# Kernel tuning notes

Hardware: AMD Instinct MI355X
Metric: run time of the kernel (lower is better)

The kernel has to match this reference:

```python
import jax, jax.numpy as jnp
import numpy as np

B, N, E, H = 2, 2048, 1024, 16
D = E // H  # head_dim = 64


def setup_inputs() -> dict:
    key = jax.random.key(0)
    ks = jax.random.split(key, 8)
    s = 1.0 / np.sqrt(D)
    return {
        "query": jax.random.normal(ks[0], (B, N, E), jnp.float32),
        "key": jax.random.normal(ks[1], (B, N, E), jnp.float32),
        "value": jax.random.normal(ks[2], (B, N, E), jnp.float32),
        "mask": jax.random.randint(ks[3], (B, N), 0, 2, jnp.int32),
        # per-head Linear weights, torch layout (out_features, in_features) stacked over heads
        "Wq": jax.random.uniform(ks[4], (H, D, D), jnp.float32, -s, s),
        "Wk": jax.random.uniform(ks[5], (H, D, D), jnp.float32, -s, s),
        "Wv": jax.random.uniform(ks[6], (H, D, D), jnp.float32, -s, s),
        "Wo": jax.random.uniform(ks[7], (E, E), jnp.float32, -1.0 / np.sqrt(E), 1.0 / np.sqrt(E)),
    }


def reference(query, key, value, mask, Wq, Wk, Wv, Wo):
    b, n, e = query.shape
    h, d, _ = Wq.shape
    q = query.reshape(b, n, h, d)
    k = key.reshape(b, n, h, d)
    v = value.reshape(b, n, h, d)
    # per-head Linear (no bias): x @ W[i].T, batched over heads
    qh = jnp.einsum('bnhd,hed->bnhe', q, Wq)
    kh = jnp.einsum('bnhd,hed->bnhe', k, Wk)
    vh = jnp.einsum('bnhd,hed->bnhe', v, Wv)
    # NOTE: original scales by sqrt(embed_size), not sqrt(head_dim)
    scores = jnp.einsum('bqhd,bkhd->bhqk', qh, kh) / (e ** 0.5)
    # NOTE: mask is unsqueezed on the KEY axis position in torch (dim=2),
    # so it masks entire QUERY rows, broadcasting over keys.
    scores = jnp.where(mask[:, None, :, None] == 0, jnp.float32(-1e28), scores)
    probs = jax.nn.softmax(scores, axis=-1)
    attn = jnp.einsum('bhqk,bkhd->bqhd', probs, vh).reshape(b, n, e)
    return attn @ Wo.T
```

## Files before the change

kernel.cpp:

```cpp
#include <hip/hip_runtime.h>
#include <hip/hip_bf16.h>

#define B_ 2
#define N_ 2048
#define E_ 1024
#define H_ 16
#define D_ 64
#define BH_ (B_ * H_)

typedef __attribute__((ext_vector_type(4))) float f32x4;
typedef __attribute__((ext_vector_type(8))) short bf16x8;
typedef __attribute__((ext_vector_type(4))) short s16x4;
typedef __attribute__((ext_vector_type(4))) int i32x4;
typedef __attribute__((ext_vector_type(2))) int i32x2;

#define MFMA(a, b, c) __builtin_amdgcn_mfma_f32_16x16x32_bf16(a, b, c, 0, 0, 0)

#define AS1(p) ((const __attribute__((address_space(1))) unsigned int*)(p))
#define AS3(p) ((__attribute__((address_space(3))) unsigned int*)(p))

static __device__ __forceinline__ unsigned short f2bf(float f) {
    unsigned int u = __builtin_bit_cast(unsigned int, f);
    u += 0x7fff + ((u >> 16) & 1);
    return (unsigned short)(u >> 16);
}
static __device__ __forceinline__ int pack2bf(float lo, float hi) {
    __hip_bfloat162 t = __float22bfloat162_rn(float2{lo, hi});
    int r;
    __builtin_memcpy(&r, &t, 4);
    return r;
}
static __device__ __forceinline__ bf16x8 cvt8s(const float* __restrict__ p, float sc) {
    f32x4 a = *(const f32x4*)p;
    f32x4 b = *(const f32x4*)(p + 4);
    i32x4 r = {pack2bf(a.x * sc, a.y * sc), pack2bf(a.z * sc, a.w * sc),
               pack2bf(b.x * sc, b.y * sc), pack2bf(b.z * sc, b.w * sc)};
    return __builtin_bit_cast(bf16x8, r);
}

__global__ __launch_bounds__(256, 4)
void proj_kernel(const float* __restrict__ q, const float* __restrict__ k,
                 const float* __restrict__ v,
                 const float* __restrict__ Wq, const float* __restrict__ Wk,
                 const float* __restrict__ Wv,
                 const int* __restrict__ mask,
                 unsigned short* __restrict__ qh, unsigned short* __restrict__ kh,
                 unsigned short* __restrict__ vt) {
    const int z = blockIdx.z;
    const float* X = (z == 0) ? q : (z == 1) ? k : v;
    const float* W = (z == 0) ? Wq : (z == 1) ? Wk : Wv;
    unsigned short* out = (z == 0) ? qh : (z == 1) ? kh : vt;
    const float wscale = (z == 0) ? (1.44269504f * 0.03125f) : 1.0f;

    const int lane = threadIdx.x & 63;
    const int wave = threadIdx.x >> 6;
    const int l16  = lane & 15;
    const int quad = lane >> 4;
    const int bh = blockIdx.y;
    const int b = bh >> 4, h = bh & 15;
    const int n0 = blockIdx.x * 64;
    const int tok = n0 + wave * 16 + l16;

    const float* xrow = X + ((size_t)(b * N_ + tok)) * E_ + h * 64;
    bf16x8 xf[2];
    xf[0] = cvt8s(xrow + quad * 8, 1.0f);
    xf[1] = cvt8s(xrow + 32 + quad * 8, 1.0f);

    const float* Wh = W + (size_t)h * 64 * 64;
    bf16x8 wf[4][2];
#pragma unroll
    for (int t4 = 0; t4 < 4; ++t4) {
        const float* wrow = Wh + (t4 * 16 + l16) * 64;
        wf[t4][0] = cvt8s(wrow + quad * 8, wscale);
        wf[t4][1] = cvt8s(wrow + 32 + quad * 8, wscale);
    }

    const int mk = (z == 0) ? mask[b * N_ + tok] : 1;

#pragma unroll
    for (int mi = 0; mi < 4; ++mi) {
        f32x4 a = {0.f, 0.f, 0.f, 0.f};
        a = MFMA(wf[mi][0], xf[0], a);
        a = MFMA(wf[mi][1], xf[1], a);
        if (z != 2) {
            i32x2 pk = {pack2bf(a.x, a.y), pack2bf(a.z, a.w)};
            if (!mk) pk = (i32x2){0, 0};
            *(i32x2*)(out + ((size_t)bh * N_ + tok) * 64 + mi * 16 + quad * 4) = pk;
        } else {
#pragma unroll
            for (int r = 0; r < 4; ++r) {
                int dout = mi * 16 + quad * 4 + r;
                out[((size_t)bh * 64 + dout) * N_ + tok] = (unsigned short)f2bf(a[r]);
            }
        }
    }
}

__global__ __launch_bounds__(256)
void cvt_wo_kernel(const float* __restrict__ wo, unsigned short* __restrict__ wob) {
    int idx = blockIdx.x * 256 + threadIdx.x;
    f32x4 v = *(const f32x4*)(wo + (size_t)idx * 4);
    i32x2 r = {pack2bf(v.x, v.y), pack2bf(v.z, v.w)};
    *(i32x2*)(wob + (size_t)idx * 4) = r;
}

__global__ __launch_bounds__(256, 2)
void attn_kernel(const unsigned short* __restrict__ qh,
                 const unsigned short* __restrict__ kh,
                 const unsigned short* __restrict__ vt,
                 unsigned short* __restrict__ attnb) {
    __shared__ short Kb[2][64][72];
    __shared__ short Vb[3][64][72];

    const int tid  = threadIdx.x;
    const int lane = tid & 63;
    const int wave = tid >> 6;
    const int l16  = lane & 15;
    const int quad = lane >> 4;

    const int flat = blockIdx.y * gridDim.x + blockIdx.x;
    const int qblk = flat >> 5;
    const int rem  = flat & 31;
    const int bh   = ((rem & 7) << 2) | (rem >> 3);
    const int b = bh >> 4, h = bh & 15;
    const int q0 = qblk * 128 + wave * 32;

    const unsigned short* kbase = kh + (size_t)bh * N_ * 64;
    const unsigned short* vbase = vt + (size_t)bh * 64 * N_;

    const int c0i = tid;
    const int c1i = tid + 256;
    const int o0 = (c0i >> 3) * 72 + (c0i & 7) * 8;
    const int o1 = (c1i >> 3) * 72 + (c1i & 7) * 8;

    short* kcur  = &Kb[0][0][0];
    short* knext = &Kb[1][0][0];
    short* vprev = &Vb[2][0][0];
    short* vcur  = &Vb[0][0][0];
    short* vnext = &Vb[1][0][0];

    const int srcA = (((quad * 2) & 3) << 4) + l16;
    const int srcB = (((quad * 2 + 1) & 3) << 4) + l16;
    const bool hiSel = (quad >= 2);

    bf16x8 qf[2][2];
#pragma unroll
    for (int qi = 0; qi < 2; ++qi) {
        const unsigned short* qrow = qh + ((size_t)bh * N_ + q0 + qi * 16 + l16) * 64;
        qf[qi][0] = *(const bf16x8*)(qrow + quad * 8);
        qf[qi][1] = *(const bf16x8*)(qrow + 32 + quad * 8);
    }

    float lI[2] = {0.f, 0.f};
    f32x4 o[4][2];
#pragma unroll
    for (int mi = 0; mi < 4; ++mi)
#pragma unroll
        for (int qi = 0; qi < 2; ++qi) o[mi][qi] = (f32x4){0.f, 0.f, 0.f, 0.f};

    bf16x8 pb[2][2];

    bf16x8 gK0, gK1, gV0, gV1;
    gK0 = *(const bf16x8*)(kbase + c0i * 8);
    gK1 = *(const bf16x8*)(kbase + c1i * 8);
    gV0 = *(const bf16x8*)(vbase + (size_t)(c0i >> 3) * N_ + (c0i & 7) * 8);
    gV1 = *(const bf16x8*)(vbase + (size_t)(c1i >> 3) * N_ + (c1i & 7) * 8);
    *(bf16x8*)(kcur + o0) = gK0;
    *(bf16x8*)(kcur + o1) = gK1;
    *(bf16x8*)(vcur + o0) = gV0;
    *(bf16x8*)(vcur + o1) = gV1;
    __syncthreads();

    for (int kt = 0; kt < N_ / 64; ++kt) {
        if (kt + 1 < N_ / 64) {
            const int k0n = (kt + 1) * 64;
            gK0 = *(const bf16x8*)(kbase + (size_t)k0n * 64 + c0i * 8);
            gK1 = *(const bf16x8*)(kbase + (size_t)k0n * 64 + c1i * 8);
            gV0 = *(const bf16x8*)(vbase + (size_t)(c0i >> 3) * N_ + k0n + (c0i & 7) * 8);
            gV1 = *(const bf16x8*)(vbase + (size_t)(c1i >> 3) * N_ + k0n + (c1i & 7) * 8);
        }

        bf16x8 ka[4][2];
#pragma unroll
        for (int t4 = 0; t4 < 4; ++t4) {
            ka[t4][0] = *(const bf16x8*)(kcur + (t4 * 16 + l16) * 72 + quad * 8);
            ka[t4][1] = *(const bf16x8*)(kcur + (t4 * 16 + l16) * 72 + 32 + quad * 8);
        }

        f32x4 s[2][4];
#pragma unroll
        for (int qi = 0; qi < 2; ++qi)
#pragma unroll
            for (int t4 = 0; t4 < 4; ++t4) {
                f32x4 z = {0.f, 0.f, 0.f, 0.f};
                z = MFMA(ka[t4][0], qf[qi][0], z);
                z = MFMA(ka[t4][1], qf[qi][1], z);
                s[qi][t4] = z;
            }

        if (kt > 0) {
            bf16x8 va[4][2];
#pragma unroll
            for (int mi = 0; mi < 4; ++mi) {
                va[mi][0] = *(const bf16x8*)(vprev + (mi * 16 + l16) * 72 + quad * 8);
                va[mi][1] = *(const bf16x8*)(vprev + (mi * 16 + l16) * 72 + 32 + quad * 8);
            }
#pragma unroll
            for (int mi = 0; mi < 4; ++mi)
#pragma unroll
                for (int qi = 0; qi < 2; ++qi) {
                    o[mi][qi] = MFMA(va[mi][0], pb[qi][0], o[mi][qi]);
                    o[mi][qi] = MFMA(va[mi][1], pb[qi][1], o[mi][qi]);
                }
        }

#pragma unroll
        for (int qi = 0; qi < 2; ++qi) {
            float rsum = 0.f;
            int pk[4][2];
#pragma unroll
            for (int t4 = 0; t4 < 4; ++t4) {
                f32x4 p;
#pragma unroll
                for (int r = 0; r < 4; ++r) {
                    p[r] = __builtin_amdgcn_exp2f(s[qi][t4][r]);
                    rsum += p[r];
                }
                pk[t4][0] = pack2bf(p.x, p.y);
                pk[t4][1] = pack2bf(p.z, p.w);
            }
            rsum += __shfl_xor(rsum, 16);
            rsum += __shfl_xor(rsum, 32);
            lI[qi] += rsum;

            i32x4 w0, w1;
#pragma unroll
            for (int d = 0; d < 2; ++d) {
                int a0 = __shfl(pk[0][d], srcA), a1 = __shfl(pk[1][d], srcA);
                int b0 = __shfl(pk[0][d], srcB), b1 = __shfl(pk[1][d], srcB);
                w0[d]     = hiSel ? a1 : a0;
                w0[2 + d] = hiSel ? b1 : b0;
                int c0 = __shfl(pk[2][d], srcA), c1 = __shfl(pk[3][d], srcA);
                int e0 = __shfl(pk[2][d], srcB), e1 = __shfl(pk[3][d], srcB);
                w1[d]     = hiSel ? c1 : c0;
                w1[2 + d] = hiSel ? e1 : e0;
            }
            pb[qi][0] = __builtin_bit_cast(bf16x8, w0);
            pb[qi][1] = __builtin_bit_cast(bf16x8, w1);
        }

        if (kt + 1 < N_ / 64) {
            *(bf16x8*)(knext + o0) = gK0;
            *(bf16x8*)(knext + o1) = gK1;
            *(bf16x8*)(vnext + o0) = gV0;
            *(bf16x8*)(vnext + o1) = gV1;
            __syncthreads();
        }

        short* t = kcur; kcur = knext; knext = t;
        short* tv = vprev; vprev = vcur; vcur = vnext; vnext = tv;
    }

    {
        bf16x8 va[4][2];
#pragma unroll
        for (int mi = 0; mi < 4; ++mi) {
            va[mi][0] = *(const bf16x8*)(vprev + (mi * 16 + l16) * 72 + quad * 8);
            va[mi][1] = *(const bf16x8*)(vprev + (mi * 16 + l16) * 72 + 32 + quad * 8);
        }
#pragma unroll
        for (int mi = 0; mi < 4; ++mi)
#pragma unroll
            for (int qi = 0; qi < 2; ++qi) {
                o[mi][qi] = MFMA(va[mi][0], pb[qi][0], o[mi][qi]);
                o[mi][qi] = MFMA(va[mi][1], pb[qi][1], o[mi][qi]);
            }
    }

#pragma unroll
    for (int qi = 0; qi < 2; ++qi) {
        const float inv = 1.0f / lI[qi];
        const int qrow_idx = q0 + qi * 16 + l16;
#pragma unroll
        for (int mi = 0; mi < 4; ++mi) {
            f32x4 ov = o[mi][qi];
            i32x2 pkk = {pack2bf(ov.x * inv, ov.y * inv),
                         pack2bf(ov.z * inv, ov.w * inv)};
            int d0 = mi * 16 + quad * 4;
            *(i32x2*)(attnb + ((size_t)(b * N_ + qrow_idx)) * E_ + h * 64 + d0) = pkk;
        }
    }
}

__global__ __launch_bounds__(512, 1)
void out_gemm_kernel(const unsigned short* __restrict__ A,
                     const unsigned short* __restrict__ Bw,
                     float* __restrict__ out) {
    __shared__ short As[2][128 * 32];
    __shared__ short Bs[2][128 * 32];

    const int tid  = threadIdx.x;
    const int lane = tid & 63;
    const int l16  = lane & 15;
    const int quad = lane >> 4;
    const int wave = tid >> 6;
    const int wm = wave & 1, wn = wave >> 1;
    const int m0 = blockIdx.x * 128;
    const int n0 = blockIdx.y * 128;

    const unsigned short* gA = A + (size_t)m0 * E_;
    const unsigned short* gB = Bw + (size_t)n0 * E_;

    f32x4 acc[4][2];
#pragma unroll
    for (int mt = 0; mt < 4; ++mt)
#pragma unroll
        for (int nt = 0; nt < 2; ++nt) acc[mt][nt] = (f32x4){0.f, 0.f, 0.f, 0.f};

    const int cc = tid >> 7, rr = tid & 127;
#define OG_STAGE(buf, k0)                                                        \
    {                                                                            \
        __builtin_amdgcn_global_load_lds(AS1(gA + (size_t)rr * E_ + (k0) + cc * 8), \
                                         AS3(&As[buf][tid * 8]), 16, 0, 0);      \
        __builtin_amdgcn_global_load_lds(AS1(gB + (size_t)rr * E_ + (k0) + cc * 8), \
                                         AS3(&Bs[buf][tid * 8]), 16, 0, 0);      \
    }

    OG_STAGE(0, 0)
    __syncthreads();

    for (int kt = 0; kt < E_ / 32; ++kt) {
        const int cur = kt & 1;
        if (kt + 1 < E_ / 32) OG_STAGE(cur ^ 1, (kt + 1) * 32)

        bf16x8 af[4], bf[2];
#pragma unroll
        for (int mt = 0; mt < 4; ++mt)
            af[mt] = *(const bf16x8*)(&As[cur][(quad * 128 + wm * 64 + mt * 16 + l16) * 8]);
#pragma unroll
        for (int nt = 0; nt < 2; ++nt)
            bf[nt] = *(const bf16x8*)(&Bs[cur][(quad * 128 + wn * 32 + nt * 16 + l16) * 8]);

#pragma unroll
        for (int mt = 0; mt < 4; ++mt)
#pragma unroll
            for (int nt = 0; nt < 2; ++nt)
                acc[mt][nt] = MFMA(af[mt], bf[nt], acc[mt][nt]);

        __syncthreads();
    }

#pragma unroll
    for (int mt = 0; mt < 4; ++mt)
#pragma unroll
        for (int nt = 0; nt < 2; ++nt)
#pragma unroll
            for (int r = 0; r < 4; ++r)
                out[(size_t)(m0 + wm * 64 + mt * 16 + quad * 4 + r) * E_ +
                    n0 + wn * 32 + nt * 16 + l16] = acc[mt][nt][r];
#undef OG_STAGE
}

extern "C" void kernel_launch(void* const* d_in, const int* in_sizes, int n_in,
                              void* d_out, int out_size, void* d_ws, size_t ws_size,
                              hipStream_t stream) {
    const float* q    = (const float*)d_in[0];
    const float* k    = (const float*)d_in[1];
    const float* v    = (const float*)d_in[2];
    const int*   mask = (const int*)d_in[3];
    const float* Wq   = (const float*)d_in[4];
    const float* Wk   = (const float*)d_in[5];
    const float* Wv   = (const float*)d_in[6];
    const float* Wo   = (const float*)d_in[7];
    float* out = (float*)d_out;

    char* ws = (char*)d_ws;
    unsigned short* qh    = (unsigned short*)(ws);
    unsigned short* kh    = (unsigned short*)(ws + (size_t)8 * 1024 * 1024);
    unsigned short* vt    = (unsigned short*)(ws + (size_t)16 * 1024 * 1024);
    unsigned short* attnb = (unsigned short*)(ws + (size_t)24 * 1024 * 1024);
    unsigned short* wob   = (unsigned short*)(ws);

    dim3 blk(256);
    proj_kernel<<<dim3(N_ / 64, BH_, 3), blk, 0, stream>>>(q, k, v, Wq, Wk, Wv, mask,
                                                           qh, kh, vt);
    attn_kernel<<<dim3(16, 32), blk, 0, stream>>>(qh, kh, vt, attnb);
    cvt_wo_kernel<<<dim3(E_ * E_ / 1024), blk, 0, stream>>>(Wo, wob);
    out_gemm_kernel<<<dim3(32, 8), dim3(512), 0, stream>>>(attnb, wob, out);
}
```

Measured before the change: 222.3 us.

## Load K and V fragments directly from global memory, dropping LDS staging

Removes the shared-memory K/V tiles and the per-iteration __syncthreads. Each wave now loads its MFMA fragments straight from global memory, prefetching the next K tile into registers. The software pipeline that deferred the PV product by one iteration is also removed, so PV runs in the same iteration. This cuts LDS traffic and block barriers, but each of the four waves now fetches the same K/V data separately from global/L2. The V loads are strided by N and now sit on the critical path inside the iteration.

```diff
diff --git a/kernel.cpp b/kernel.cpp
--- a/kernel.cpp
+++ b/kernel.cpp
@@ -109,9 +109,6 @@
                  const unsigned short* __restrict__ kh,
                  const unsigned short* __restrict__ vt,
                  unsigned short* __restrict__ attnb) {
-    __shared__ short Kb[2][64][72];
-    __shared__ short Vb[3][64][72];
-
     const int tid  = threadIdx.x;
     const int lane = tid & 63;
     const int wave = tid >> 6;
@@ -125,19 +122,8 @@
     const int b = bh >> 4, h = bh & 15;
     const int q0 = qblk * 128 + wave * 32;
 
-    const unsigned short* kbase = kh + (size_t)bh * N_ * 64;
-    const unsigned short* vbase = vt + (size_t)bh * 64 * N_;
-
-    const int c0i = tid;
-    const int c1i = tid + 256;
-    const int o0 = (c0i >> 3) * 72 + (c0i & 7) * 8;
-    const int o1 = (c1i >> 3) * 72 + (c1i & 7) * 8;
-
-    short* kcur  = &Kb[0][0][0];
-    short* knext = &Kb[1][0][0];
-    short* vprev = &Vb[2][0][0];
-    short* vcur  = &Vb[0][0][0];
-    short* vnext = &Vb[1][0][0];
+    const unsigned short* kp = kh + (size_t)bh * N_ * 64 + l16 * 64 + quad * 8;
+    const unsigned short* vp = vt + (size_t)bh * 64 * N_ + (size_t)l16 * N_ + quad * 8;
 
     const int srcA = (((quad * 2) & 3) << 4) + l16;
     const int srcB = (((quad * 2 + 1) & 3) << 4) + l16;
@@ -158,33 +144,30 @@
 #pragma unroll
         for (int qi = 0; qi < 2; ++qi) o[mi][qi] = (f32x4){0.f, 0.f, 0.f, 0.f};
 
-    bf16x8 pb[2][2];
-
-    bf16x8 gK0, gK1, gV0, gV1;
-    gK0 = *(const bf16x8*)(kbase + c0i * 8);
-    gK1 = *(const bf16x8*)(kbase + c1i * 8);
-    gV0 = *(const bf16x8*)(vbase + (size_t)(c0i >> 3) * N_ + (c0i & 7) * 8);
-    gV1 = *(const bf16x8*)(vbase + (size_t)(c1i >> 3) * N_ + (c1i & 7) * 8);
-    *(bf16x8*)(kcur + o0) = gK0;
-    *(bf16x8*)(kcur + o1) = gK1;
-    *(bf16x8*)(vcur + o0) = gV0;
-    *(bf16x8*)(vcur + o1) = gV1;
-    __syncthreads();
+    bf16x8 ka[4][2];
+#pragma unroll
+    for (int t4 = 0; t4 < 4; ++t4) {
+        ka[t4][0] = *(const bf16x8*)(kp + (size_t)(t4 * 16) * 64);
+        ka[t4][1] = *(const bf16x8*)(kp + (size_t)(t4 * 16) * 64 + 32);
+    }
 
     for (int kt = 0; kt < N_ / 64; ++kt) {
+        bf16x8 kan[4][2];
         if (kt + 1 < N_ / 64) {
-            const int k0n = (kt + 1) * 64;
-            gK0 = *(const bf16x8*)(kbase + (size_t)k0n * 64 + c0i * 8);
-            gK1 = *(const bf16x8*)(kbase + (size_t)k0n * 64 + c1i * 8);
-            gV0 = *(const bf16x8*)(vbase + (size_t)(c0i >> 3) * N_ + k0n + (c0i & 7) * 8);
-            gV1 = *(const bf16x8*)(vbase + (size_t)(c1i >> 3) * N_ + k0n + (c1i & 7) * 8);
-        }
-
-        bf16x8 ka[4][2];
-#pragma unroll
-        for (int t4 = 0; t4 < 4; ++t4) {
-            ka[t4][0] = *(const bf16x8*)(kcur + (t4 * 16 + l16) * 72 + quad * 8);
-            ka[t4][1] = *(const bf16x8*)(kcur + (t4 * 16 + l16) * 72 + 32 + quad * 8);
+            const unsigned short* kpn = kp + (size_t)(kt + 1) * 64 * 64;
+#pragma unroll
+            for (int t4 = 0; t4 < 4; ++t4) {
+                kan[t4][0] = *(const bf16x8*)(kpn + (size_t)(t4 * 16) * 64);
+                kan[t4][1] = *(const bf16x8*)(kpn + (size_t)(t4 * 16) * 64 + 32);
+            }
+        }
+
+        bf16x8 va[4][2];
+#pragma unroll
+        for (int mi = 0; mi < 4; ++mi) {
+            const unsigned short* vrow = vp + (size_t)(mi * 16) * N_ + kt * 64;
+            va[mi][0] = *(const bf16x8*)(vrow);
+            va[mi][1] = *(const bf16x8*)(vrow + 32);
         }
 
         f32x4 s[2][4];
@@ -197,22 +180,6 @@
                 z = MFMA(ka[t4][1], qf[qi][1], z);
                 s[qi][t4] = z;
             }
-
-        if (kt > 0) {
-            bf16x8 va[4][2];
-#pragma unroll
-            for (int mi = 0; mi < 4; ++mi) {
-                va[mi][0] = *(const bf16x8*)(vprev + (mi * 16 + l16) * 72 + quad * 8);
-                va[mi][1] = *(const bf16x8*)(vprev + (mi * 16 + l16) * 72 + 32 + quad * 8);
-            }
-#pragma unroll
-            for (int mi = 0; mi < 4; ++mi)
-#pragma unroll
-                for (int qi = 0; qi < 2; ++qi) {
-                    o[mi][qi] = MFMA(va[mi][0], pb[qi][0], o[mi][qi]);
-                    o[mi][qi] = MFMA(va[mi][1], pb[qi][1], o[mi][qi]);
-                }
-        }
 
 #pragma unroll
         for (int qi = 0; qi < 2; ++qi) {
@@ -245,36 +212,21 @@
                 w1[d]     = hiSel ? c1 : c0;
                 w1[2 + d] = hiSel ? e1 : e0;
             }
-            pb[qi][0] = __builtin_bit_cast(bf16x8, w0);
-            pb[qi][1] = __builtin_bit_cast(bf16x8, w1);
-        }
-
-        if (kt + 1 < N_ / 64) {
-            *(bf16x8*)(knext + o0) = gK0;
-            *(bf16x8*)(knext + o1) = gK1;
-            *(bf16x8*)(vnext + o0) = gV0;
-            *(bf16x8*)(vnext + o1) = gV1;
-            __syncthreads();
-        }
-
-        short* t = kcur; kcur = knext; knext = t;
-        short* tv = vprev; vprev = vcur; vcur = vnext; vnext = tv;
-    }
-
-    {
-        bf16x8 va[4][2];
-#pragma unroll
-        for (int mi = 0; mi < 4; ++mi) {
-            va[mi][0] = *(const bf16x8*)(vprev + (mi * 16 + l16) * 72 + quad * 8);
-            va[mi][1] = *(const bf16x8*)(vprev + (mi * 16 + l16) * 72 + 32 + quad * 8);
-        }
-#pragma unroll
-        for (int mi = 0; mi < 4; ++mi)
-#pragma unroll
-            for (int qi = 0; qi < 2; ++qi) {
-                o[mi][qi] = MFMA(va[mi][0], pb[qi][0], o[mi][qi]);
-                o[mi][qi] = MFMA(va[mi][1], pb[qi][1], o[mi][qi]);
-            }
+            bf16x8 pb0 = __builtin_bit_cast(bf16x8, w0);
+            bf16x8 pb1 = __builtin_bit_cast(bf16x8, w1);
+
+#pragma unroll
+            for (int mi = 0; mi < 4; ++mi) {
+                o[mi][qi] = MFMA(va[mi][0], pb0, o[mi][qi]);
+                o[mi][qi] = MFMA(va[mi][1], pb1, o[mi][qi]);
+            }
+        }
+
+#pragma unroll
+        for (int t4 = 0; t4 < 4; ++t4) {
+            ka[t4][0] = kan[t4][0];
+            ka[t4][1] = kan[t4][1];
+        }
     }
 
 #pragma unroll
```

New measurement: 275.0 us. 1.24x slower.

## Use fp16 16x16x16 MFMA for PV to drop cross-lane P shuffles

Applied to the files above, without the earlier changes.

Stores V transposed in fp16 and switches the P·V product to the 16x16x16 f16 MFMA, whose operand layout matches the score accumulator layout. This removes the per-tile __shfl permutation of probabilities. The row-sum reduction is deferred to the end, accumulating per-lane vectors. The change doubles the PV MFMA instruction count at half the K-depth, pads the V LDS rows to 76 and uses round-toward-zero fp16 conversion for P, which changes precision slightly.

```diff
diff --git a/kernel.cpp b/kernel.cpp
--- a/kernel.cpp
+++ b/kernel.cpp
@@ -13,8 +13,10 @@
 typedef __attribute__((ext_vector_type(4))) short s16x4;
 typedef __attribute__((ext_vector_type(4))) int i32x4;
 typedef __attribute__((ext_vector_type(2))) int i32x2;
+typedef __attribute__((ext_vector_type(4))) _Float16 f16x4;
 
 #define MFMA(a, b, c) __builtin_amdgcn_mfma_f32_16x16x32_bf16(a, b, c, 0, 0, 0)
+#define MFMA16(a, b, c) __builtin_amdgcn_mfma_f32_16x16x16f16(a, b, c, 0, 0, 0)
 
 #define AS1(p) ((const __attribute__((address_space(1))) unsigned int*)(p))
 #define AS3(p) ((__attribute__((address_space(3))) unsigned int*)(p))
@@ -36,6 +38,14 @@
     i32x4 r = {pack2bf(a.x * sc, a.y * sc), pack2bf(a.z * sc, a.w * sc),
                pack2bf(b.x * sc, b.y * sc), pack2bf(b.z * sc, b.w * sc)};
     return __builtin_bit_cast(bf16x8, r);
+}
+static __device__ __forceinline__ f16x4 pack4f16(f32x4 p) {
+    auto lo = __builtin_amdgcn_cvt_pkrtz(p.x, p.y);
+    auto hi = __builtin_amdgcn_cvt_pkrtz(p.z, p.w);
+    f16x4 r;
+    __builtin_memcpy(&r, &lo, 4);
+    __builtin_memcpy(((char*)&r) + 4, &hi, 4);
+    return r;
 }
 
 __global__ __launch_bounds__(256, 4)
@@ -90,7 +100,10 @@
 #pragma unroll
             for (int r = 0; r < 4; ++r) {
                 int dout = mi * 16 + quad * 4 + r;
-                out[((size_t)bh * 64 + dout) * N_ + tok] = (unsigned short)f2bf(a[r]);
+                _Float16 hv = (_Float16)a[r];
+                unsigned short us;
+                __builtin_memcpy(&us, &hv, 2);
+                out[((size_t)bh * 64 + dout) * N_ + tok] = us;
             }
         }
     }
@@ -109,8 +122,8 @@
                  const unsigned short* __restrict__ kh,
                  const unsigned short* __restrict__ vt,
                  unsigned short* __restrict__ attnb) {
-    __shared__ short Kb[2][64][72];
-    __shared__ short Vb[3][64][72];
+    __shared__ short Kb[2][64 * 72];
+    __shared__ short Vb[3][64 * 76];
 
     const int tid  = threadIdx.x;
     const int lane = tid & 63;
@@ -130,18 +143,16 @@
 
     const int c0i = tid;
     const int c1i = tid + 256;
-    const int o0 = (c0i >> 3) * 72 + (c0i & 7) * 8;
-    const int o1 = (c1i >> 3) * 72 + (c1i & 7) * 8;
-
-    short* kcur  = &Kb[0][0][0];
-    short* knext = &Kb[1][0][0];
-    short* vprev = &Vb[2][0][0];
-    short* vcur  = &Vb[0][0][0];
-    short* vnext = &Vb[1][0][0];
-
-    const int srcA = (((quad * 2) & 3) << 4) + l16;
-    const int srcB = (((quad * 2 + 1) & 3) << 4) + l16;
-    const bool hiSel = (quad >= 2);
+    const int k0o = (c0i >> 3) * 72 + (c0i & 7) * 8;
+    const int k1o = (c1i >> 3) * 72 + (c1i & 7) * 8;
+    const int v0o = (c0i >> 3) * 76 + (c0i & 7) * 8;
+    const int v1o = (c1i >> 3) * 76 + (c1i & 7) * 8;
+
+    short* kcur  = &Kb[0][0];
+    short* knext = &Kb[1][0];
+    short* vprev = &Vb[2][0];
+    short* vcur  = &Vb[0][0];
+    short* vnext = &Vb[1][0];
 
     bf16x8 qf[2][2];
 #pragma unroll
@@ -151,24 +162,24 @@
         qf[qi][1] = *(const bf16x8*)(qrow + 32 + quad * 8);
     }
 
-    float lI[2] = {0.f, 0.f};
+    f32x4 psum[2] = {{0.f, 0.f, 0.f, 0.f}, {0.f, 0.f, 0.f, 0.f}};
     f32x4 o[4][2];
 #pragma unroll
     for (int mi = 0; mi < 4; ++mi)
 #pragma unroll
         for (int qi = 0; qi < 2; ++qi) o[mi][qi] = (f32x4){0.f, 0.f, 0.f, 0.f};
 
-    bf16x8 pb[2][2];
+    f16x4 pf[2][4];
 
     bf16x8 gK0, gK1, gV0, gV1;
     gK0 = *(const bf16x8*)(kbase + c0i * 8);
     gK1 = *(const bf16x8*)(kbase + c1i * 8);
     gV0 = *(const bf16x8*)(vbase + (size_t)(c0i >> 3) * N_ + (c0i & 7) * 8);
     gV1 = *(const bf16x8*)(vbase + (size_t)(c1i >> 3) * N_ + (c1i & 7) * 8);
-    *(bf16x8*)(kcur + o0) = gK0;
-    *(bf16x8*)(kcur + o1) = gK1;
-    *(bf16x8*)(vcur + o0) = gV0;
-    *(bf16x8*)(vcur + o1) = gV1;
+    *(bf16x8*)(kcur + k0o) = gK0;
+    *(bf16x8*)(kcur + k1o) = gK1;
+    *(bf16x8*)(vcur + v0o) = gV0;
+    *(bf16x8*)(vcur + v1o) = gV1;
     __syncthreads();
 
     for (int kt = 0; kt < N_ / 64; ++kt) {
@@ -186,7 +197,6 @@
             ka[t4][0] = *(const bf16x8*)(kcur + (t4 * 16 + l16) * 72 + quad * 8);
             ka[t4][1] = *(const bf16x8*)(kcur + (t4 * 16 + l16) * 72 + 32 + quad * 8);
         }
-
         f32x4 s[2][4];
 #pragma unroll
         for (int qi = 0; qi < 2; ++qi)
@@ -199,61 +209,36 @@
             }
 
         if (kt > 0) {
-            bf16x8 va[4][2];
 #pragma unroll
             for (int mi = 0; mi < 4; ++mi) {
-                va[mi][0] = *(const bf16x8*)(vprev + (mi * 16 + l16) * 72 + quad * 8);
-                va[mi][1] = *(const bf16x8*)(vprev + (mi * 16 + l16) * 72 + 32 + quad * 8);
+#pragma unroll
+                for (int t4 = 0; t4 < 4; ++t4) {
+                    f16x4 va = *(const f16x4*)(vprev + (mi * 16 + l16) * 76 +
+                                               t4 * 16 + quad * 4);
+#pragma unroll
+                    for (int qi = 0; qi < 2; ++qi)
+                        o[mi][qi] = MFMA16(va, pf[qi][t4], o[mi][qi]);
+                }
             }
-#pragma unroll
-            for (int mi = 0; mi < 4; ++mi)
-#pragma unroll
-                for (int qi = 0; qi < 2; ++qi) {
-                    o[mi][qi] = MFMA(va[mi][0], pb[qi][0], o[mi][qi]);
-                    o[mi][qi] = MFMA(va[mi][1], pb[qi][1], o[mi][qi]);
-                }
         }
 
 #pragma unroll
         for (int qi = 0; qi < 2; ++qi) {
-            float rsum = 0.f;
-            int pk[4][2];
 #pragma unroll
             for (int t4 = 0; t4 < 4; ++t4) {
                 f32x4 p;
 #pragma unroll
-                for (int r = 0; r < 4; ++r) {
-                    p[r] = __builtin_amdgcn_exp2f(s[qi][t4][r]);
-                    rsum += p[r];
-                }
-                pk[t4][0] = pack2bf(p.x, p.y);
-                pk[t4][1] = pack2bf(p.z, p.w);
+                for (int r = 0; r < 4; ++r) p[r] = __builtin_amdgcn_exp2f(s[qi][t4][r]);
+                psum[qi] += p;
+                pf[qi][t4] = pack4f16(p);
             }
-            rsum += __shfl_xor(rsum, 16);
-            rsum += __shfl_xor(rsum, 32);
-            lI[qi] += rsum;
-
-            i32x4 w0, w1;
-#pragma unroll
-            for (int d = 0; d < 2; ++d) {
-                int a0 = __shfl(pk[0][d], srcA), a1 = __shfl(pk[1][d], srcA);
-                int b0 = __shfl(pk[0][d], srcB), b1 = __shfl(pk[1][d], srcB);
-                w0[d]     = hiSel ? a1 : a0;
-                w0[2 + d] = hiSel ? b1 : b0;
-                int c0 = __shfl(pk[2][d], srcA), c1 = __shfl(pk[3][d], srcA);
-                int e0 = __shfl(pk[2][d], srcB), e1 = __shfl(pk[3][d], srcB);
-                w1[d]     = hiSel ? c1 : c0;
-                w1[2 + d] = hiSel ? e1 : e0;
-            }
-            pb[qi][0] = __builtin_bit_cast(bf16x8, w0);
-            pb[qi][1] = __builtin_bit_cast(bf16x8, w1);
         }
 
         if (kt + 1 < N_ / 64) {
-            *(bf16x8*)(knext + o0) = gK0;
-            *(bf16x8*)(knext + o1) = gK1;
-            *(bf16x8*)(vnext + o0) = gV0;
-            *(bf16x8*)(vnext + o1) = gV1;
+            *(bf16x8*)(knext + k0o) = gK0;
+            *(bf16x8*)(knext + k1o) = gK1;
+            *(bf16x8*)(vnext + v0o) = gV0;
+            *(bf16x8*)(vnext + v1o) = gV1;
             __syncthreads();
         }
 
@@ -261,25 +246,24 @@
         short* tv = vprev; vprev = vcur; vcur = vnext; vnext = tv;
     }
 
-    {
-        bf16x8 va[4][2];
-#pragma unroll
-        for (int mi = 0; mi < 4; ++mi) {
-            va[mi][0] = *(const bf16x8*)(vprev + (mi * 16 + l16) * 72 + quad * 8);
-            va[mi][1] = *(const bf16x8*)(vprev + (mi * 16 + l16) * 72 + 32 + quad * 8);
-        }
-#pragma unroll
-        for (int mi = 0; mi < 4; ++mi)
-#pragma unroll
-            for (int qi = 0; qi < 2; ++qi) {
-                o[mi][qi] = MFMA(va[mi][0], pb[qi][0], o[mi][qi]);
-                o[mi][qi] = MFMA(va[mi][1], pb[qi][1], o[mi][qi]);
-            }
+#pragma unroll
+    for (int mi = 0; mi < 4; ++mi) {
+#pragma unroll
+        for (int t4 = 0; t4 < 4; ++t4) {
+            f16x4 va = *(const f16x4*)(vprev + (mi * 16 + l16) * 76 +
+                                       t4 * 16 + quad * 4);
+#pragma unroll
+            for (int qi = 0; qi < 2; ++qi)
+                o[mi][qi] = MFMA16(va, pf[qi][t4], o[mi][qi]);
+        }
     }
 
 #pragma unroll
     for (int qi = 0; qi < 2; ++qi) {
-        const float inv = 1.0f / lI[qi];
+        float rs = psum[qi].x + psum[qi].y + psum[qi].z + psum[qi].w;
+        rs += __shfl_xor(rs, 16);
+        rs += __shfl_xor(rs, 32);
+        const float inv = 1.0f / rs;
         const int qrow_idx = q0 + qi * 16 + l16;
 #pragma unroll
         for (int mi = 0; mi < 4; ++mi) {
```

Result: faster. 199.9 us (-10.1%).
